# Optimization experiments

Measured on AMD Instinct MI355X. Metric: run time of the kernel, lower is better.

Reference implementation:

```python
import jax, jax.numpy as jnp
import numpy as np

N_EVENT = 100000
N_TRACE = 20000
E_EE = 1000000
E_ET = 500000
E_TE = 500000
D = 128          # embedding_dim == hidden_dim
OUT = 64         # output_dim
L = 3            # num_layers
NTYPES_EDGES = 3 # edge types
B = 64           # graphs per batch


def setup_inputs() -> dict:
    key = jax.random.key(0)
    ks = jax.random.split(key, 16)
    s = 1.0 / np.sqrt(D)
    inp = {
        "event_ids": jnp.arange(N_EVENT, dtype=jnp.int64 if jax.config.jax_enable_x64 else jnp.int32),
        "trace_ids": jnp.arange(N_TRACE, dtype=jnp.int64 if jax.config.jax_enable_x64 else jnp.int32),
        "e2e_src": jax.random.randint(ks[0], (E_EE,), 0, N_EVENT),
        "e2e_dst": jax.random.randint(ks[1], (E_EE,), 0, N_EVENT),
        "e2t_src": jax.random.randint(ks[2], (E_ET,), 0, N_EVENT),
        "e2t_dst": jax.random.randint(ks[3], (E_ET,), 0, N_TRACE),
        "t2e_src": jax.random.randint(ks[4], (E_TE,), 0, N_TRACE),
        "t2e_dst": jax.random.randint(ks[5], (E_TE,), 0, N_EVENT),
        "event_batch": jnp.sort(jax.random.randint(ks[6], (N_EVENT,), 0, B)),
        "trace_batch": jnp.sort(jax.random.randint(ks[7], (N_TRACE,), 0, B)),
        # learned parameters
        "emb_event": jax.random.normal(ks[8], (N_EVENT, D), jnp.float32),
        "emb_trace": jax.random.normal(ks[9], (N_TRACE, D), jnp.float32),
        # per-layer, per-edge-type SAGEConv weights: lin_l (neighbor, with bias), lin_r (root, no bias)
        "Wl": jax.random.normal(ks[10], (L, NTYPES_EDGES, D, D), jnp.float32) * s,
        "bl": jnp.zeros((L, NTYPES_EDGES, D), jnp.float32),
        "Wr": jax.random.normal(ks[11], (L, NTYPES_EDGES, D, D), jnp.float32) * s,
        # output MLP head
        "W1": jax.random.normal(ks[12], (D, D), jnp.float32) * s,
        "b1": jnp.zeros((D,), jnp.float32),
        "W2": jax.random.normal(ks[13], (OUT, D), jnp.float32) * s,
        "b2": jnp.zeros((OUT,), jnp.float32),
    }
    return inp


def reference(event_ids, trace_ids, e2e_src, e2e_dst, e2t_src, e2t_dst,
              t2e_src, t2e_dst, event_batch, trace_batch,
              emb_event, emb_trace, Wl, bl, Wr, W1, b1, W2, b2):
    def seg_mean(x_src, src, dst, n_dst):
        # mean-aggregate source features onto destination nodes (SAGEConv default aggr)
        s = jax.ops.segment_sum(x_src[src], dst, num_segments=n_dst)
        c = jax.ops.segment_sum(jnp.ones(dst.shape, x_src.dtype), dst, num_segments=n_dst)
        return s / jnp.maximum(c, 1.0)[:, None]

    # per-node-type embedding lookup
    x = {"event": emb_event[event_ids], "trace": emb_trace[trace_ids]}
    n = {"event": event_ids.shape[0], "trace": trace_ids.shape[0]}
    # edge types: (src_type, dst_type, src_idx, dst_idx), conv index matches Wl/bl/Wr axis 1
    edges = [
        ("event", "event", e2e_src, e2e_dst),
        ("event", "trace", e2t_src, e2t_dst),
        ("trace", "event", t2e_src, t2e_dst),
    ]
    n_layers = Wl.shape[0]
    for l in range(n_layers):
        new = {k: jnp.zeros((n[k], Wl.shape[-2]), x[k].dtype) for k in x}
        for i, (st, dt, s_idx, d_idx) in enumerate(edges):
            m = seg_mean(x[st], s_idx, d_idx, n[dt])
            # SAGEConv: lin_l(mean neighbors) + lin_r(root); HeteroConv aggr='sum' across edge types
            new[dt] = new[dt] + m @ Wl[l, i].T + bl[l, i] + x[dt] @ Wr[l, i].T
        x = new
    # global_add_pool per node type, then stack+sum over node types
    pooled = (jax.ops.segment_sum(x["event"], event_batch, num_segments=B)
              + jax.ops.segment_sum(x["trace"], trace_batch, num_segments=B))
    h = jax.nn.relu(pooled @ W1.T + b1)
    return h @ W2.T + b2
```

## Files before the change

### kernel.cpp

```cpp
#include <hip/hip_runtime.h>
#include <hip/hip_bf16.h>


#define D 128
#define NB 64
#define OUTD 64
#define NLAY 3
#define EPB 4096
#define BSH2 9

typedef __bf16 bf16;
typedef __bf16 bf16x4 __attribute__((ext_vector_type(4)));
typedef __bf16 bf16x8 __attribute__((ext_vector_type(8)));
typedef float  f32x16 __attribute__((ext_vector_type(16)));

#define LOAD16_TO_LDS(gp, lp) \
    __builtin_amdgcn_global_load_lds((const __attribute__((address_space(1))) void*)(gp), \
                                     (__attribute__((address_space(3))) void*)(lp), 16, 0, 0)

__global__ void gather_all(const float* __restrict__ embE, const int* __restrict__ idsE,
                           bf16* __restrict__ xE, int nE,
                           const float* __restrict__ embT, const int* __restrict__ idsT,
                           bf16* __restrict__ xT, int nT) {
    int idx = blockIdx.x * blockDim.x + threadIdx.x;
    const float* emb; const int* ids; bf16* x;
    int tE = nE * 32;
    if (idx < tE) { emb = embE; ids = idsE; x = xE; }
    else {
        idx -= tE;
        if (idx >= nT * 32) return;
        emb = embT; ids = idsT; x = xT;
    }
    int r = idx >> 5, v = idx & 31;
    float4 f = ((const float4*)(emb + (size_t)ids[r] * D))[v];
    bf16x4 o;
    o[0] = (bf16)f.x; o[1] = (bf16)f.y; o[2] = (bf16)f.z; o[3] = (bf16)f.w;
    ((bf16x4*)(x + (size_t)r * D))[v] = o;
}

__global__ void bkt_hist_all(const int* __restrict__ dEE, int nEE, int nbkEE, int nblkEE,
                             int* __restrict__ cntEE,
                             const int* __restrict__ dET, int nET, int nbkET, int nblkET,
                             int* __restrict__ cntET,
                             const int* __restrict__ dTE, int nTE, int nbkTE, int nblkTE,
                             int* __restrict__ cntTE) {
    __shared__ int h[256];
    int b = blockIdx.x;
    const int* dst; int E, nbk, nblk, lb; int* cnt;
    if (b < nblkEE) { dst = dEE; E = nEE; nbk = nbkEE; nblk = nblkEE; cnt = cntEE; lb = b; }
    else if (b < nblkEE + nblkET) { dst = dET; E = nET; nbk = nbkET; nblk = nblkET; cnt = cntET; lb = b - nblkEE; }
    else { dst = dTE; E = nTE; nbk = nbkTE; nblk = nblkTE; cnt = cntTE; lb = b - nblkEE - nblkET; }
    h[threadIdx.x] = 0;
    __syncthreads();
    int e0 = lb * EPB, e1 = min(e0 + EPB, E);
    for (int e = e0 + threadIdx.x; e < e1; e += 256) atomicAdd(&h[dst[e] >> BSH2], 1);
    __syncthreads();
    for (int k = threadIdx.x; k < nbk; k += 256) cnt[k * nblk + lb] = h[k];
}

__global__ void scan_p1_all(const int* __restrict__ dA, int* __restrict__ oA, int* __restrict__ sA, int nA,
                            const int* __restrict__ dB, int* __restrict__ oB, int* __restrict__ sB, int nB,
                            const int* __restrict__ dC, int* __restrict__ oC, int* __restrict__ sC, int nC) {
    int nbA = (nA + 1023) >> 10, nbB = (nB + 1023) >> 10;
    int b = blockIdx.x;
    const int* deg; int* off; int* bsum; int n; int lb;
    if (b < nbA) { deg = dA; off = oA; bsum = sA; n = nA; lb = b; }
    else if (b < nbA + nbB) { deg = dB; off = oB; bsum = sB; n = nB; lb = b - nbA; }
    else { deg = dC; off = oC; bsum = sC; n = nC; lb = b - nbA - nbB; }
    __shared__ int s[256];
    int t = threadIdx.x;
    int base = lb * 1024 + t * 4;
    int v[4];
    #pragma unroll
    for (int i = 0; i < 4; ++i) v[i] = (base + i < n) ? deg[base + i] : 0;
    int tot = v[0] + v[1] + v[2] + v[3];
    s[t] = tot;
    __syncthreads();
    for (int st = 1; st < 256; st <<= 1) {
        int x = (t >= st) ? s[t - st] : 0;
        __syncthreads();
        s[t] += x;
        __syncthreads();
    }
    int run = s[t] - tot;
    #pragma unroll
    for (int i = 0; i < 4; ++i) {
        if (base + i < n) off[base + i] = run;
        run += v[i];
    }
    if (t == 255) bsum[lb] = s[255];
}

__global__ void scan_p2_all(int* __restrict__ sA, int nbA,
                            int* __restrict__ sB, int nbB,
                            int* __restrict__ sC, int nbC) {
    int* bsum; int nb;
    if (blockIdx.x == 0) { bsum = sA; nb = nbA; }
    else if (blockIdx.x == 1) { bsum = sB; nb = nbB; }
    else { bsum = sC; nb = nbC; }
    __shared__ int s[256];
    int t = threadIdx.x;
    int v = (t < nb) ? bsum[t] : 0;
    s[t] = v;
    __syncthreads();
    for (int st = 1; st < 256; st <<= 1) {
        int x = (t >= st) ? s[t - st] : 0;
        __syncthreads();
        s[t] += x;
        __syncthreads();
    }
    if (t < nb) bsum[t] = s[t] - v;
    if (t == 0) bsum[nb] = s[255];
}

__global__ void scan_p3_all(int* __restrict__ oA, const int* __restrict__ sA, int nA,
                            int* __restrict__ oB, const int* __restrict__ sB, int nB,
                            int* __restrict__ oC, const int* __restrict__ sC, int nC) {
    int cbA = (nA + 255) >> 8, cbB = (nB + 255) >> 8;
    int b = blockIdx.x;
    int* off; const int* bsum; int n; int lb;
    if (b < cbA) { off = oA; bsum = sA; n = nA; lb = b; }
    else if (b < cbA + cbB) { off = oB; bsum = sB; n = nB; lb = b - cbA; }
    else { off = oC; bsum = sC; n = nC; lb = b - cbA - cbB; }
    int i = lb * 256 + threadIdx.x;
    if (i < n) off[i] += bsum[i >> 10];
    if (i == 0) off[n] = bsum[(n + 1023) >> 10];
}

__global__ void bkt_scatter_all(const int* __restrict__ sEE, const int* __restrict__ dEE,
                                int nEE, int nbkEE, int nblkEE, const int* __restrict__ SEE,
                                int2* __restrict__ ebEE,
                                const int* __restrict__ sET, const int* __restrict__ dET,
                                int nET, int nbkET, int nblkET, const int* __restrict__ SET,
                                int2* __restrict__ ebET,
                                const int* __restrict__ sTE, const int* __restrict__ dTE,
                                int nTE, int nbkTE, int nblkTE, const int* __restrict__ STE,
                                int2* __restrict__ ebTE) {
    __shared__ int cu[256];
    int b = blockIdx.x;
    const int* src; const int* dst; const int* S; int2* eb; int E, nbk, nblk, lb;
    if (b < nblkEE) { src = sEE; dst = dEE; S = SEE; eb = ebEE; E = nEE; nbk = nbkEE; nblk = nblkEE; lb = b; }
    else if (b < nblkEE + nblkET) { src = sET; dst = dET; S = SET; eb = ebET; E = nET; nbk = nbkET; nblk = nblkET; lb = b - nblkEE; }
    else { src = sTE; dst = dTE; S = STE; eb = ebTE; E = nTE; nbk = nbkTE; nblk = nblkTE; lb = b - nblkEE - nblkET; }
    for (int k = threadIdx.x; k < nbk; k += 256) cu[k] = S[k * nblk + lb];
    __syncthreads();
    int e0 = lb * EPB, e1 = min(e0 + EPB, E);
    for (int e = e0 + threadIdx.x; e < e1; e += 256) {
        int s = src[e], d = dst[e];
        int p = atomicAdd(&cu[d >> BSH2], 1);
        eb[p] = make_int2(s, d);
    }
}

__global__ void csr_build_all(const int2* __restrict__ ebEE, const int* __restrict__ SEE,
                              int nbkEE, int nblkEE, int ndEE,
                              int* __restrict__ offEE, int* __restrict__ adjEE,
                              const int2* __restrict__ ebET, const int* __restrict__ SET,
                              int nbkET, int nblkET, int ndET,
                              int* __restrict__ offET, int* __restrict__ adjET,
                              const int2* __restrict__ ebTE, const int* __restrict__ STE,
                              int nbkTE, int nblkTE, int ndTE,
                              int* __restrict__ offTE, int* __restrict__ adjTE) {
    __shared__ int h[512];
    __shared__ int ps[256];
    __shared__ int cc[512];
    int b = blockIdx.x;
    const int2* eb; const int* S; int nbk, nblk, ndst, k; int* off; int* adj;
    if (b < nbkEE) { eb = ebEE; S = SEE; nbk = nbkEE; nblk = nblkEE; ndst = ndEE; off = offEE; adj = adjEE; k = b; }
    else if (b < nbkEE + nbkET) { eb = ebET; S = SET; nbk = nbkET; nblk = nblkET; ndst = ndET; off = offET; adj = adjET; k = b - nbkEE; }
    else { eb = ebTE; S = STE; nbk = nbkTE; nblk = nblkTE; ndst = ndTE; off = offTE; adj = adjTE; k = b - nbkEE - nbkET; }
    int base = S[k * nblk];
    int end  = (k == nbk - 1) ? S[nbk * nblk] : S[(k + 1) * nblk];
    int d0 = k << BSH2;
    int t = threadIdx.x;
    h[t] = 0; h[t + 256] = 0;
    __syncthreads();
    for (int j = base + t; j < end; j += 256) atomicAdd(&h[eb[j].y - d0], 1);
    __syncthreads();
    int a0 = h[2 * t], a1 = h[2 * t + 1];
    ps[t] = a0 + a1;
    __syncthreads();
    for (int st = 1; st < 256; st <<= 1) {
        int x = (t >= st) ? ps[t - st] : 0;
        __syncthreads();
        ps[t] += x;
        __syncthreads();
    }
    int pe = ps[t] - (a0 + a1);
    int o0 = base + pe, o1 = base + pe + a0;
    cc[2 * t] = o0; cc[2 * t + 1] = o1;
    int nd = min(512, ndst - d0);
    if (2 * t < nd) off[d0 + 2 * t] = o0;
    if (2 * t + 1 < nd) off[d0 + 2 * t + 1] = o1;
    if (t == 0 && k == nbk - 1) off[ndst] = end;
    __syncthreads();
    for (int j = base + t; j < end; j += 256) {
        int2 e = eb[j];
        int p = atomicAdd(&cc[e.y - d0], 1);
        adj[p] = e.x;
    }
}

__global__ void agg_all(const bf16* __restrict__ xE, const bf16* __restrict__ xT,
                        const int* __restrict__ offEE, const int* __restrict__ adjEE,
                        const int* __restrict__ offTE, const int* __restrict__ adjTE,
                        const int* __restrict__ offET, const int* __restrict__ adjET,
                        bf16* __restrict__ mEE, bf16* __restrict__ mTE, bf16* __restrict__ mET,
                        int nE, int nT) {
    int gw = (blockIdx.x * blockDim.x + threadIdx.x) >> 6;
    int lane = threadIdx.x & 63;
    int qE = (nE + 3) >> 2, qT = (nT + 3) >> 2;
    const bf16* xsrc; const int* off; const int* adj; bf16* out; int ndst;
    if (gw < qE) { xsrc = xE; off = offEE; adj = adjEE; out = mEE; ndst = nE; }
    else if (gw < 2 * qE) { gw -= qE; xsrc = xT; off = offTE; adj = adjTE; out = mTE; ndst = nE; }
    else {
        gw -= 2 * qE;
        if (gw >= qT) return;
        xsrc = xE; off = offET; adj = adjET; out = mET; ndst = nT;
    }
    int sub = lane >> 4;
    int sl  = lane & 15;
    int row = gw * 4 + sub;
    if (row >= ndst) row = ndst - 1;
    int s0 = off[row], s1 = off[row + 1];
    float a[8] = {};
    int j = s0;
    for (; j + 8 <= s1; j += 8) {
        int ii[8];
        #pragma unroll
        for (int u = 0; u < 8; ++u) ii[u] = adj[j + u];
        bf16x8 v[8];
        #pragma unroll
        for (int u = 0; u < 8; ++u) v[u] = ((const bf16x8*)(xsrc + (size_t)ii[u] * D))[sl];
        #pragma unroll
        for (int u = 0; u < 8; ++u)
            #pragma unroll
            for (int e = 0; e < 8; ++e) a[e] += (float)v[u][e];
    }
    for (; j + 4 <= s1; j += 4) {
        int i0 = adj[j], i1 = adj[j + 1], i2 = adj[j + 2], i3 = adj[j + 3];
        bf16x8 v0 = ((const bf16x8*)(xsrc + (size_t)i0 * D))[sl];
        bf16x8 v1 = ((const bf16x8*)(xsrc + (size_t)i1 * D))[sl];
        bf16x8 v2 = ((const bf16x8*)(xsrc + (size_t)i2 * D))[sl];
        bf16x8 v3 = ((const bf16x8*)(xsrc + (size_t)i3 * D))[sl];
        #pragma unroll
        for (int e = 0; e < 8; ++e)
            a[e] += (float)v0[e] + (float)v1[e] + (float)v2[e] + (float)v3[e];
    }
    for (; j < s1; ++j) {
        int i0 = adj[j];
        bf16x8 v0 = ((const bf16x8*)(xsrc + (size_t)i0 * D))[sl];
        #pragma unroll
        for (int e = 0; e < 8; ++e) a[e] += (float)v0[e];
    }
    float inv = 1.0f / fmaxf((float)(s1 - s0), 1.0f);
    bf16x8 o;
    #pragma unroll
    for (int e = 0; e < 8; ++e) o[e] = (bf16)(a[e] * inv);
    ((bf16x8*)(out + (size_t)row * D))[sl] = o;
}

__global__ void prep_weights_packed(const float* __restrict__ Wl, const float* __restrict__ Wr,
                                    bf16* __restrict__ wbuf) {
    int idx = blockIdx.x * blockDim.x + threadIdx.x;
    if (idx >= NLAY * 5 * 2048) return;
    int l = idx / (5 * 2048);
    int rem = idx - l * 5 * 2048;
    int mat = rem >> 11;
    int q = rem & 2047;
    int lane = q & 63, t = (q >> 6) & 7, w = q >> 9;
    int r = w * 32 + (lane & 31);
    int c = t * 16 + (lane >> 5) * 8;
    size_t l3 = (size_t)l * 3;
    const float* s0;
    const float* s1 = nullptr;
    switch (mat) {
        case 0: s0 = Wl + (l3 + 0) * D * D; break;
        case 1: s0 = Wl + (l3 + 2) * D * D; break;
        case 2: s0 = Wr + (l3 + 0) * D * D; s1 = Wr + (l3 + 2) * D * D; break;
        case 3: s0 = Wl + (l3 + 1) * D * D; break;
        default: s0 = Wr + (l3 + 1) * D * D; break;
    }
    bf16x8 hi, lo;
    #pragma unroll
    for (int e = 0; e < 8; ++e) {
        float v = s0[r * D + c + e];
        if (s1) v += s1[r * D + c + e];
        bf16 h = (bf16)v;
        hi[e] = h;
        lo[e] = (bf16)(v - (float)h);
    }
    bf16* base = wbuf + (size_t)l * 10 * D * D;
    ((bf16x8*)(base + (size_t)(2 * mat) * D * D))[q] = hi;
    ((bf16x8*)(base + (size_t)(2 * mat + 1) * D * D))[q] = lo;
}

__global__ void prep_bias(const float* __restrict__ bl, float* __restrict__ bbuf) {
    int idx = blockIdx.x * blockDim.x + threadIdx.x;
    if (idx >= NLAY * D) return;
    int l = idx >> 7, o = idx & (D - 1);
    bbuf[l * 2 * D + o]     = bl[(size_t)(l * 3 + 0) * D + o] + bl[(size_t)(l * 3 + 2) * D + o];
    bbuf[l * 2 * D + D + o] = bl[(size_t)(l * 3 + 1) * D + o];
}

__device__ __forceinline__ void gemm_body(const bf16* A0, const bf16* A1, const bf16* A2,
                                          const bf16* Wp, const float* bias, bf16* out,
                                          int M, int nm, int row0, bf16* As) {
    int tid = threadIdx.x;
    int wave = tid >> 6, lane = tid & 63;
    int m = lane & 31, half = lane >> 5;

    f32x16 acc[2];
    #pragma unroll
    for (int rt = 0; rt < 2; ++rt)
        #pragma unroll
        for (int i = 0; i < 16; ++i) acc[rt][i] = 0.f;

    const bf16* Aptr[3] = {A0, A1, A2};
    #pragma unroll
    for (int s = 0; s < 3; ++s) {
        if (s >= nm) break;
        if (s) __syncthreads();
        const bf16* Amat = Aptr[s];
        #pragma unroll
        for (int p = 0; p < 4; ++p) {
            int si = p * 256 + tid;
            int r = si >> 4, u = si & 15;
            int gr = row0 + r; if (gr >= M) gr = M - 1;
            int gc = (u ^ (r & 15)) * 8;
            LOAD16_TO_LDS(Amat + (size_t)gr * D + gc, As + (size_t)(p * 4 + wave) * 512);
        }
        const bf16* wph = Wp + (size_t)(2 * s) * D * D + ((size_t)wave * 512 + lane) * 8;
        const bf16* wpl = wph + D * D;
        bf16x8 bh_c  = *(const bf16x8*)(wph);
        bf16x8 blo_c = *(const bf16x8*)(wpl);
        __syncthreads();

        #pragma unroll 1
        for (int t = 0; t < 8; ++t) {
            bf16x8 bh_n, blo_n;
            if (t < 7) {
                bh_n  = *(const bf16x8*)(wph + (t + 1) * 512);
                blo_n = *(const bf16x8*)(wpl + (t + 1) * 512);
            }
            bf16x8 af[2];
            #pragma unroll
            for (int rt = 0; rt < 2; ++rt) {
                int r = rt * 32 + m;
                int c = t * 2 + half;
                af[rt] = *(const bf16x8*)(As + ((size_t)r * 16 + (c ^ (r & 15))) * 8);
            }
            acc[0] = __builtin_amdgcn_mfma_f32_32x32x16_bf16(af[0], bh_c,  acc[0], 0, 0, 0);
            acc[1] = __builtin_amdgcn_mfma_f32_32x32x16_bf16(af[1], bh_c,  acc[1], 0, 0, 0);
            acc[0] = __builtin_amdgcn_mfma_f32_32x32x16_bf16(af[0], blo_c, acc[0], 0, 0, 0);
            acc[1] = __builtin_amdgcn_mfma_f32_32x32x16_bf16(af[1], blo_c, acc[1], 0, 0, 0);
            bh_c = bh_n; blo_c = blo_n;
        }
    }

    int col = wave * 32 + m;
    float bv = bias[col];
    #pragma unroll
    for (int rt = 0; rt < 2; ++rt) {
        #pragma unroll
        for (int r = 0; r < 16; ++r) {
            int row = row0 + rt * 32 + (r & 3) + 8 * (r >> 2) + 4 * half;
            if (row < M) out[(size_t)row * D + col] = (bf16)(acc[rt][r] + bv);
        }
    }
}

__global__ __launch_bounds__(256) void gemm_all(const bf16* __restrict__ eA0, const bf16* __restrict__ eA1,
                                                const bf16* __restrict__ eA2, const bf16* __restrict__ eW,
                                                const float* __restrict__ eB, bf16* __restrict__ eOut,
                                                int Me, int bE,
                                                const bf16* __restrict__ tA0, const bf16* __restrict__ tA1,
                                                const bf16* __restrict__ tW, const float* __restrict__ tB,
                                                bf16* __restrict__ tOut, int Mt) {
    __shared__ bf16 As[64 * 128];
    if ((int)blockIdx.x < bE)
        gemm_body(eA0, eA1, eA2, eW, eB, eOut, Me, 3, blockIdx.x * 64, As);
    else
        gemm_body(tA0, tA1, (const bf16*)nullptr, tW, tB, tOut, Mt, 2,
                  ((int)blockIdx.x - bE) * 64, As);
}

__global__ void pool_m_all(const bf16* __restrict__ m_ee, const bf16* __restrict__ m_te,
                           const bf16* __restrict__ xE, const bf16* __restrict__ m_et,
                           const bf16* __restrict__ xT,
                           const int* __restrict__ bEv, const int* __restrict__ bTr,
                           int nE, int nT, int pbE, int pbT,
                           float* __restrict__ pooled5, int* __restrict__ cntE,
                           int* __restrict__ cntT) {
    int c = threadIdx.x;
    int blk = blockIdx.x;
    const bf16* x; const int* batch; int n, r0, s;
    if (blk < 3 * pbE) {
        s = blk / pbE; int lb = blk - s * pbE;
        x = (s == 0) ? m_ee : (s == 1) ? m_te : xE;
        batch = bEv; n = nE; r0 = lb * 64;
    } else {
        int q = blk - 3 * pbE;
        s = 3 + q / pbT; int lb = q - (s - 3) * pbT;
        x = (s == 3) ? m_et : xT;
        batch = bTr; n = nT; r0 = lb * 64;
    }
    int r1 = min(r0 + 64, n);
    if (r0 >= r1) return;
    float* P = pooled5 + (size_t)s * NB * D;
    int* cnt = (s == 2) ? cntE : (s == 4) ? cntT : nullptr;
    int cur = batch[r0];
    float acc = 0.f;
    int run = 0;
    for (int r = r0; r < r1; ++r) {
        int b = batch[r];
        if (b != cur) {
            atomicAdd(&P[cur * D + c], acc);
            if (cnt && c == 0) atomicAdd(&cnt[cur], run);
            acc = 0.f; run = 0; cur = b;
        }
        acc += (float)x[(size_t)r * D + c];
        run++;
    }
    atomicAdd(&P[cur * D + c], acc);
    if (cnt && c == 0) atomicAdd(&cnt[cur], run);
}

__global__ void tail_kernel(const float* __restrict__ pooled5, const int* __restrict__ cntE,
                            const int* __restrict__ cntT,
                            const float* __restrict__ Wl, const float* __restrict__ Wr,
                            const float* __restrict__ bl,
                            const float* __restrict__ W1, const float* __restrict__ b1,
                            const float* __restrict__ W2, const float* __restrict__ b2,
                            float* __restrict__ out) {
    __shared__ float p5[5][D];
    __shared__ float hp[D];
    __shared__ float hh[D];
    int b = blockIdx.x, t = threadIdx.x;
    #pragma unroll
    for (int s = 0; s < 5; ++s) p5[s][t] = pooled5[(size_t)(s * NB + b) * D + t];
    __syncthreads();
    float ce = (float)cntE[b], ct = (float)cntT[b];
    float s = ce * (bl[6 * D + t] + bl[8 * D + t]) + ct * bl[7 * D + t];
    const float* w0  = Wl + (size_t)6 * D * D + (size_t)t * D;
    const float* w2  = Wl + (size_t)8 * D * D + (size_t)t * D;
    const float* wr0 = Wr + (size_t)6 * D * D + (size_t)t * D;
    const float* wr2 = Wr + (size_t)8 * D * D + (size_t)t * D;
    const float* w1m = Wl + (size_t)7 * D * D + (size_t)t * D;
    const float* wr1 = Wr + (size_t)7 * D * D + (size_t)t * D;
    #pragma unroll 4
    for (int k = 0; k < D; ++k)
        s += p5[0][k] * w0[k] + p5[1][k] * w2[k] + p5[2][k] * (wr0[k] + wr2[k])
           + p5[3][k] * w1m[k] + p5[4][k] * wr1[k];
    hp[t] = s;
    __syncthreads();
    float s1 = b1[t];
    const float* u = W1 + (size_t)t * D;
    #pragma unroll 4
    for (int k = 0; k < D; ++k) s1 += hp[k] * u[k];
    hh[t] = fmaxf(s1, 0.f);
    __syncthreads();
    if (t < OUTD) {
        float s2 = b2[t];
        const float* v = W2 + (size_t)t * D;
        #pragma unroll 4
        for (int k = 0; k < D; ++k) s2 += hh[k] * v[k];
        out[b * OUTD + t] = s2;
    }
}

extern "C" void kernel_launch(void* const* d_in, const int* in_sizes, int n_in,
                              void* d_out, int out_size, void* d_ws, size_t ws_size,
                              hipStream_t stream) {
    const int* event_ids   = (const int*)d_in[0];
    const int* trace_ids   = (const int*)d_in[1];
    const int* e2e_src     = (const int*)d_in[2];
    const int* e2e_dst     = (const int*)d_in[3];
    const int* e2t_src     = (const int*)d_in[4];
    const int* e2t_dst     = (const int*)d_in[5];
    const int* t2e_src     = (const int*)d_in[6];
    const int* t2e_dst     = (const int*)d_in[7];
    const int* event_batch = (const int*)d_in[8];
    const int* trace_batch = (const int*)d_in[9];
    const float* emb_event = (const float*)d_in[10];
    const float* emb_trace = (const float*)d_in[11];
    const float* Wl        = (const float*)d_in[12];
    const float* bl        = (const float*)d_in[13];
    const float* Wr        = (const float*)d_in[14];
    const float* W1        = (const float*)d_in[15];
    const float* b1        = (const float*)d_in[16];
    const float* W2        = (const float*)d_in[17];
    const float* b2        = (const float*)d_in[18];

    const int NE = in_sizes[0];
    const int NT = in_sizes[1];
    const int EE = in_sizes[2];
    const int ET = in_sizes[4];
    const int TE = in_sizes[6];

    const int nbkEE = (NE + 511) >> BSH2, nblkEE = (EE + EPB - 1) / EPB;
    const int nbkET = (NT + 511) >> BSH2, nblkET = (ET + EPB - 1) / EPB;
    const int nbkTE = (NE + 511) >> BSH2, nblkTE = (TE + EPB - 1) / EPB;
    const int cEE = nbkEE * nblkEE, cET = nbkET * nblkET, cTE = nbkTE * nblkTE;

    size_t cur = 0;
    auto alloc = [&](size_t bytes) -> void* {
        cur = (cur + 255) & ~(size_t)255;
        void* p = (char*)d_ws + cur;
        cur += bytes;
        return p;
    };
    bf16* x_event   = (bf16*)alloc((size_t)NE * D * 2);
    bf16* x_trace   = (bf16*)alloc((size_t)NT * D * 2);
    bf16* nx_event  = (bf16*)alloc((size_t)NE * D * 2);
    bf16* nx_trace  = (bf16*)alloc((size_t)NT * D * 2);
    bf16* m_ee      = (bf16*)alloc((size_t)NE * D * 2);
    bf16* m_te      = (bf16*)alloc((size_t)NE * D * 2);
    bf16* m_et      = (bf16*)alloc((size_t)NT * D * 2);
    bf16* wbuf      = (bf16*)alloc((size_t)NLAY * 10 * D * D * 2);
    float* bbuf     = (float*)alloc((size_t)NLAY * 2 * D * 4);
    size_t zInts = (size_t)5 * NB * D + 2 * NB;
    int* zbase  = (int*)alloc(zInts * 4);
    float* pooled5 = (float*)zbase;
    int* cntE = (int*)(pooled5 + 5 * NB * D);
    int* cntT = cntE + NB;
    int* off_ee = (int*)alloc((size_t)(NE + 1) * 4);
    int* adj_ee = (int*)alloc((size_t)EE * 4);
    int* off_et = (int*)alloc((size_t)(NT + 1) * 4);
    int* adj_et = (int*)alloc((size_t)ET * 4);
    int* off_te = (int*)alloc((size_t)(NE + 1) * 4);
    int* adj_te = (int*)alloc((size_t)TE * 4);
    int* cnt_ee = (int*)alloc((size_t)cEE * 4);
    int* S_ee   = (int*)alloc((size_t)(cEE + 1) * 4);
    int* cnt_et = (int*)alloc((size_t)cET * 4);
    int* S_et   = (int*)alloc((size_t)(cET + 1) * 4);
    int* cnt_te = (int*)alloc((size_t)cTE * 4);
    int* S_te   = (int*)alloc((size_t)(cTE + 1) * 4);
    int* bsum_ee = (int*)alloc(((size_t)(cEE + 1023) / 1024 + 1) * 4);
    int* bsum_et = (int*)alloc(((size_t)(cET + 1023) / 1024 + 1) * 4);
    int* bsum_te = (int*)alloc(((size_t)(cTE + 1023) / 1024 + 1) * 4);
    int2* eb_ee = (int2*)m_ee;
    int2* eb_et = (int2*)m_te;
    int2* eb_te = (int2*)m_et;
    (void)ws_size; (void)n_in; (void)out_size;

    hipMemsetAsync(zbase, 0, zInts * 4, stream);

    gather_all<<<((NE + NT) * 32 + 255) / 256, 256, 0, stream>>>(
        emb_event, event_ids, x_event, NE, emb_trace, trace_ids, x_trace, NT);

    prep_weights_packed<<<(NLAY * 5 * 2048 + 255) / 256, 256, 0, stream>>>(Wl, Wr, wbuf);
    prep_bias<<<(NLAY * D + 255) / 256, 256, 0, stream>>>(bl, bbuf);

    bkt_hist_all<<<nblkEE + nblkET + nblkTE, 256, 0, stream>>>(
        e2e_dst, EE, nbkEE, nblkEE, cnt_ee,
        e2t_dst, ET, nbkET, nblkET, cnt_et,
        t2e_dst, TE, nbkTE, nblkTE, cnt_te);
    const int nb1 = (cEE + 1023) >> 10, nb2 = (cET + 1023) >> 10, nb3 = (cTE + 1023) >> 10;
    scan_p1_all<<<nb1 + nb2 + nb3, 256, 0, stream>>>(
        cnt_ee, S_ee, bsum_ee, cEE, cnt_et, S_et, bsum_et, cET, cnt_te, S_te, bsum_te, cTE);
    scan_p2_all<<<3, 256, 0, stream>>>(bsum_ee, nb1, bsum_et, nb2, bsum_te, nb3);
    scan_p3_all<<<((cEE + 255) >> 8) + ((cET + 255) >> 8) + ((cTE + 255) >> 8), 256, 0, stream>>>(
        S_ee, bsum_ee, cEE, S_et, bsum_et, cET, S_te, bsum_te, cTE);
    bkt_scatter_all<<<nblkEE + nblkET + nblkTE, 256, 0, stream>>>(
        e2e_src, e2e_dst, EE, nbkEE, nblkEE, S_ee, eb_ee,
        e2t_src, e2t_dst, ET, nbkET, nblkET, S_et, eb_et,
        t2e_src, t2e_dst, TE, nbkTE, nblkTE, S_te, eb_te);
    csr_build_all<<<nbkEE + nbkET + nbkTE, 256, 0, stream>>>(
        eb_ee, S_ee, nbkEE, nblkEE, NE, off_ee, adj_ee,
        eb_et, S_et, nbkET, nblkET, NT, off_et, adj_et,
        eb_te, S_te, nbkTE, nblkTE, NE, off_te, adj_te);

    const int qE = (NE + 3) >> 2, qT = (NT + 3) >> 2;
    const int aggBlocks = (2 * qE + qT + 3) / 4;
    const int bE = (NE + 63) / 64, bT = (NT + 63) / 64;
    for (int l = 0; l < NLAY; ++l) {
        agg_all<<<aggBlocks, 256, 0, stream>>>(x_event, x_trace,
                                               off_ee, adj_ee, off_te, adj_te, off_et, adj_et,
                                               m_ee, m_te, m_et, NE, NT);
        if (l < NLAY - 1) {
            const bf16* wl_ev = wbuf + (size_t)l * 10 * D * D;
            const bf16* wl_tr = wl_ev + (size_t)6 * D * D;
            const float* be = bbuf + (size_t)l * 2 * D;
            const float* bt = be + D;
            gemm_all<<<bE + bT, 256, 0, stream>>>(m_ee, m_te, x_event, wl_ev, be, nx_event, NE, bE,
                                                  m_et, x_trace, wl_tr, bt, nx_trace, NT);
            bf16* t;
            t = x_event; x_event = nx_event; nx_event = t;
            t = x_trace; x_trace = nx_trace; nx_trace = t;
        }
    }

    const int pbE = (NE + 63) / 64, pbT = (NT + 63) / 64;
    pool_m_all<<<3 * pbE + 2 * pbT, D, 0, stream>>>(m_ee, m_te, x_event, m_et, x_trace,
                                                    event_batch, trace_batch, NE, NT, pbE, pbT,
                                                    pooled5, cntE, cntT);
    tail_kernel<<<NB, D, 0, stream>>>(pooled5, cntE, cntT, Wl, Wr, bl,
                                      W1, b1, W2, b2, (float*)d_out);
}
```

Measured before the change: 602.3 us.

## Fuse front-end prep kernels, merge scan phases, double-buffer GEMM weights, enlarge pool chunks

Folds the embedding gather, weight packing and bias prep into one launch, and merges scan phases 2 and 3 so that every block redundantly rescans the block sums. This is meant to cut kernel-launch count and the serial dependencies between tiny kernels. The GEMM inner loop is fully unrolled with a two-deep register prefetch of weight fragments, and its launch bounds now request 8 blocks per multiprocessor. Pooling chunks grow from 64 to 256 rows to reduce atomics. The costs are redundant scan work in each block and possible register pressure under the tighter launch bounds.

```diff
diff --git a/kernel.cpp b/kernel.cpp
--- a/kernel.cpp
+++ b/kernel.cpp
@@ -8,6 +8,7 @@
 #define NLAY 3
 #define EPB 4096
 #define BSH2 9
+#define PCH 256
 
 typedef __bf16 bf16;
 typedef __bf16 bf16x4 __attribute__((ext_vector_type(4)));
@@ -18,24 +19,69 @@
     __builtin_amdgcn_global_load_lds((const __attribute__((address_space(1))) void*)(gp), \
                                      (__attribute__((address_space(3))) void*)(lp), 16, 0, 0)
 
-__global__ void gather_all(const float* __restrict__ embE, const int* __restrict__ idsE,
-                           bf16* __restrict__ xE, int nE,
-                           const float* __restrict__ embT, const int* __restrict__ idsT,
-                           bf16* __restrict__ xT, int nT) {
-    int idx = blockIdx.x * blockDim.x + threadIdx.x;
-    const float* emb; const int* ids; bf16* x;
-    int tE = nE * 32;
-    if (idx < tE) { emb = embE; ids = idsE; x = xE; }
-    else {
-        idx -= tE;
-        if (idx >= nT * 32) return;
-        emb = embT; ids = idsT; x = xT;
-    }
-    int r = idx >> 5, v = idx & 31;
-    float4 f = ((const float4*)(emb + (size_t)ids[r] * D))[v];
-    bf16x4 o;
-    o[0] = (bf16)f.x; o[1] = (bf16)f.y; o[2] = (bf16)f.z; o[3] = (bf16)f.w;
-    ((bf16x4*)(x + (size_t)r * D))[v] = o;
+__global__ void front_all(const float* __restrict__ embE, const int* __restrict__ idsE,
+                          bf16* __restrict__ xE, int nE,
+                          const float* __restrict__ embT, const int* __restrict__ idsT,
+                          bf16* __restrict__ xT, int nT,
+                          const float* __restrict__ Wl, const float* __restrict__ Wr,
+                          const float* __restrict__ bl,
+                          bf16* __restrict__ wbuf, float* __restrict__ bbuf,
+                          int nGather) {
+    int b = blockIdx.x;
+    if (b < nGather) {
+        int idx = b * 256 + threadIdx.x;
+        const float* emb; const int* ids; bf16* x;
+        int tE = nE * 32;
+        if (idx < tE) { emb = embE; ids = idsE; x = xE; }
+        else {
+            idx -= tE;
+            if (idx >= nT * 32) return;
+            emb = embT; ids = idsT; x = xT;
+        }
+        int r = idx >> 5, v = idx & 31;
+        float4 f = ((const float4*)(emb + (size_t)ids[r] * D))[v];
+        bf16x4 o;
+        o[0] = (bf16)f.x; o[1] = (bf16)f.y; o[2] = (bf16)f.z; o[3] = (bf16)f.w;
+        ((bf16x4*)(x + (size_t)r * D))[v] = o;
+    } else if (b < nGather + 120) {
+        int idx = (b - nGather) * 256 + threadIdx.x;
+        if (idx >= NLAY * 5 * 2048) return;
+        int l = idx / (5 * 2048);
+        int rem = idx - l * 5 * 2048;
+        int mat = rem >> 11;
+        int q = rem & 2047;
+        int lane = q & 63, t = (q >> 6) & 7, w = q >> 9;
+        int r = w * 32 + (lane & 31);
+        int c = t * 16 + (lane >> 5) * 8;
+        size_t l3 = (size_t)l * 3;
+        const float* s0;
+        const float* s1 = nullptr;
+        switch (mat) {
+            case 0: s0 = Wl + (l3 + 0) * D * D; break;
+            case 1: s0 = Wl + (l3 + 2) * D * D; break;
+            case 2: s0 = Wr + (l3 + 0) * D * D; s1 = Wr + (l3 + 2) * D * D; break;
+            case 3: s0 = Wl + (l3 + 1) * D * D; break;
+            default: s0 = Wr + (l3 + 1) * D * D; break;
+        }
+        bf16x8 hi, lo;
+        #pragma unroll
+        for (int e = 0; e < 8; ++e) {
+            float v = s0[r * D + c + e];
+            if (s1) v += s1[r * D + c + e];
+            bf16 h = (bf16)v;
+            hi[e] = h;
+            lo[e] = (bf16)(v - (float)h);
+        }
+        bf16* base = wbuf + (size_t)l * 10 * D * D;
+        ((bf16x8*)(base + (size_t)(2 * mat) * D * D))[q] = hi;
+        ((bf16x8*)(base + (size_t)(2 * mat + 1) * D * D))[q] = lo;
+    } else {
+        int idx = (b - nGather - 120) * 256 + threadIdx.x;
+        if (idx >= NLAY * D) return;
+        int l = idx >> 7, o = idx & (D - 1);
+        bbuf[l * 2 * D + o]     = bl[(size_t)(l * 3 + 0) * D + o] + bl[(size_t)(l * 3 + 2) * D + o];
+        bbuf[l * 2 * D + D + o] = bl[(size_t)(l * 3 + 1) * D + o];
+    }
 }
 
 __global__ void bkt_hist_all(const int* __restrict__ dEE, int nEE, int nbkEE, int nblkEE,
@@ -91,40 +137,33 @@
     if (t == 255) bsum[lb] = s[255];
 }
 
-__global__ void scan_p2_all(int* __restrict__ sA, int nbA,
-                            int* __restrict__ sB, int nbB,
-                            int* __restrict__ sC, int nbC) {
-    int* bsum; int nb;
-    if (blockIdx.x == 0) { bsum = sA; nb = nbA; }
-    else if (blockIdx.x == 1) { bsum = sB; nb = nbB; }
-    else { bsum = sC; nb = nbC; }
-    __shared__ int s[256];
-    int t = threadIdx.x;
-    int v = (t < nb) ? bsum[t] : 0;
-    s[t] = v;
-    __syncthreads();
-    for (int st = 1; st < 256; st <<= 1) {
-        int x = (t >= st) ? s[t - st] : 0;
-        __syncthreads();
-        s[t] += x;
-        __syncthreads();
-    }
-    if (t < nb) bsum[t] = s[t] - v;
-    if (t == 0) bsum[nb] = s[255];
-}
-
-__global__ void scan_p3_all(int* __restrict__ oA, const int* __restrict__ sA, int nA,
-                            int* __restrict__ oB, const int* __restrict__ sB, int nB,
-                            int* __restrict__ oC, const int* __restrict__ sC, int nC) {
+__global__ void scan_p23_all(int* __restrict__ oA, const int* __restrict__ sA, int nA,
+                             int* __restrict__ oB, const int* __restrict__ sB, int nB,
+                             int* __restrict__ oC, const int* __restrict__ sC, int nC) {
     int cbA = (nA + 255) >> 8, cbB = (nB + 255) >> 8;
     int b = blockIdx.x;
     int* off; const int* bsum; int n; int lb;
     if (b < cbA) { off = oA; bsum = sA; n = nA; lb = b; }
     else if (b < cbA + cbB) { off = oB; bsum = sB; n = nB; lb = b - cbA; }
     else { off = oC; bsum = sC; n = nC; lb = b - cbA - cbB; }
-    int i = lb * 256 + threadIdx.x;
-    if (i < n) off[i] += bsum[i >> 10];
-    if (i == 0) off[n] = bsum[(n + 1023) >> 10];
+    __shared__ int s[256];
+    __shared__ int ex[256];
+    int nb = (n + 1023) >> 10;
+    int t = threadIdx.x;
+    int v = (t < nb) ? bsum[t] : 0;
+    s[t] = v;
+    __syncthreads();
+    for (int st = 1; st < 256; st <<= 1) {
+        int x = (t >= st) ? s[t - st] : 0;
+        __syncthreads();
+        s[t] += x;
+        __syncthreads();
+    }
+    ex[t] = s[t] - v;
+    __syncthreads();
+    int i = lb * 256 + t;
+    if (i < n) off[i] += ex[i >> 10];
+    if (i == 0) off[n] = s[nb - 1];
 }
 
 __global__ void bkt_scatter_all(const int* __restrict__ sEE, const int* __restrict__ dEE,
@@ -260,49 +299,6 @@
     ((bf16x8*)(out + (size_t)row * D))[sl] = o;
 }
 
-__global__ void prep_weights_packed(const float* __restrict__ Wl, const float* __restrict__ Wr,
-                                    bf16* __restrict__ wbuf) {
-    int idx = blockIdx.x * blockDim.x + threadIdx.x;
-    if (idx >= NLAY * 5 * 2048) return;
-    int l = idx / (5 * 2048);
-    int rem = idx - l * 5 * 2048;
-    int mat = rem >> 11;
-    int q = rem & 2047;
-    int lane = q & 63, t = (q >> 6) & 7, w = q >> 9;
-    int r = w * 32 + (lane & 31);
-    int c = t * 16 + (lane >> 5) * 8;
-    size_t l3 = (size_t)l * 3;
-    const float* s0;
-    const float* s1 = nullptr;
-    switch (mat) {
-        case 0: s0 = Wl + (l3 + 0) * D * D; break;
-        case 1: s0 = Wl + (l3 + 2) * D * D; break;
-        case 2: s0 = Wr + (l3 + 0) * D * D; s1 = Wr + (l3 + 2) * D * D; break;
-        case 3: s0 = Wl + (l3 + 1) * D * D; break;
-        default: s0 = Wr + (l3 + 1) * D * D; break;
-    }
-    bf16x8 hi, lo;
-    #pragma unroll
-    for (int e = 0; e < 8; ++e) {
-        float v = s0[r * D + c + e];
-        if (s1) v += s1[r * D + c + e];
-        bf16 h = (bf16)v;
-        hi[e] = h;
-        lo[e] = (bf16)(v - (float)h);
-    }
-    bf16* base = wbuf + (size_t)l * 10 * D * D;
-    ((bf16x8*)(base + (size_t)(2 * mat) * D * D))[q] = hi;
-    ((bf16x8*)(base + (size_t)(2 * mat + 1) * D * D))[q] = lo;
-}
-
-__global__ void prep_bias(const float* __restrict__ bl, float* __restrict__ bbuf) {
-    int idx = blockIdx.x * blockDim.x + threadIdx.x;
-    if (idx >= NLAY * D) return;
-    int l = idx >> 7, o = idx & (D - 1);
-    bbuf[l * 2 * D + o]     = bl[(size_t)(l * 3 + 0) * D + o] + bl[(size_t)(l * 3 + 2) * D + o];
-    bbuf[l * 2 * D + D + o] = bl[(size_t)(l * 3 + 1) * D + o];
-}
-
 __device__ __forceinline__ void gemm_body(const bf16* A0, const bf16* A1, const bf16* A2,
                                           const bf16* Wp, const float* bias, bf16* out,
                                           int M, int nm, int row0, bf16* As) {
@@ -332,16 +328,19 @@
         }
         const bf16* wph = Wp + (size_t)(2 * s) * D * D + ((size_t)wave * 512 + lane) * 8;
         const bf16* wpl = wph + D * D;
-        bf16x8 bh_c  = *(const bf16x8*)(wph);
-        bf16x8 blo_c = *(const bf16x8*)(wpl);
-        __syncthreads();
-
-        #pragma unroll 1
+        bf16x8 bh0 = *(const bf16x8*)(wph);
+        bf16x8 bl0 = *(const bf16x8*)(wpl);
+        bf16x8 bh1 = *(const bf16x8*)(wph + 512);
+        bf16x8 bl1 = *(const bf16x8*)(wpl + 512);
+        __syncthreads();
+
+        #pragma unroll
         for (int t = 0; t < 8; ++t) {
-            bf16x8 bh_n, blo_n;
-            if (t < 7) {
-                bh_n  = *(const bf16x8*)(wph + (t + 1) * 512);
-                blo_n = *(const bf16x8*)(wpl + (t + 1) * 512);
+            bf16x8 bhc = (t & 1) ? bh1 : bh0;
+            bf16x8 blc = (t & 1) ? bl1 : bl0;
+            if (t < 6) {
+                if (t & 1) { bh1 = *(const bf16x8*)(wph + (t + 2) * 512); bl1 = *(const bf16x8*)(wpl + (t + 2) * 512); }
+                else       { bh0 = *(const bf16x8*)(wph + (t + 2) * 512); bl0 = *(const bf16x8*)(wpl + (t + 2) * 512); }
             }
             bf16x8 af[2];
             #pragma unroll
@@ -350,11 +349,10 @@
                 int c = t * 2 + half;
                 af[rt] = *(const bf16x8*)(As + ((size_t)r * 16 + (c ^ (r & 15))) * 8);
             }
-            acc[0] = __builtin_amdgcn_mfma_f32_32x32x16_bf16(af[0], bh_c,  acc[0], 0, 0, 0);
-            acc[1] = __builtin_amdgcn_mfma_f32_32x32x16_bf16(af[1], bh_c,  acc[1], 0, 0, 0);
-            acc[0] = __builtin_amdgcn_mfma_f32_32x32x16_bf16(af[0], blo_c, acc[0], 0, 0, 0);
-            acc[1] = __builtin_amdgcn_mfma_f32_32x32x16_bf16(af[1], blo_c, acc[1], 0, 0, 0);
-            bh_c = bh_n; blo_c = blo_n;
+            acc[0] = __builtin_amdgcn_mfma_f32_32x32x16_bf16(af[0], bhc, acc[0], 0, 0, 0);
+            acc[1] = __builtin_amdgcn_mfma_f32_32x32x16_bf16(af[1], bhc, acc[1], 0, 0, 0);
+            acc[0] = __builtin_amdgcn_mfma_f32_32x32x16_bf16(af[0], blc, acc[0], 0, 0, 0);
+            acc[1] = __builtin_amdgcn_mfma_f32_32x32x16_bf16(af[1], blc, acc[1], 0, 0, 0);
         }
     }
 
@@ -370,13 +368,13 @@
     }
 }
 
-__global__ __launch_bounds__(256) void gemm_all(const bf16* __restrict__ eA0, const bf16* __restrict__ eA1,
-                                                const bf16* __restrict__ eA2, const bf16* __restrict__ eW,
-                                                const float* __restrict__ eB, bf16* __restrict__ eOut,
-                                                int Me, int bE,
-                                                const bf16* __restrict__ tA0, const bf16* __restrict__ tA1,
-                                                const bf16* __restrict__ tW, const float* __restrict__ tB,
-                                                bf16* __restrict__ tOut, int Mt) {
+__global__ __launch_bounds__(256, 8) void gemm_all(const bf16* __restrict__ eA0, const bf16* __restrict__ eA1,
+                                                   const bf16* __restrict__ eA2, const bf16* __restrict__ eW,
+                                                   const float* __restrict__ eB, bf16* __restrict__ eOut,
+                                                   int Me, int bE,
+                                                   const bf16* __restrict__ tA0, const bf16* __restrict__ tA1,
+                                                   const bf16* __restrict__ tW, const float* __restrict__ tB,
+                                                   bf16* __restrict__ tOut, int Mt) {
     __shared__ bf16 As[64 * 128];
     if ((int)blockIdx.x < bE)
         gemm_body(eA0, eA1, eA2, eW, eB, eOut, Me, 3, blockIdx.x * 64, As);
@@ -398,14 +396,14 @@
     if (blk < 3 * pbE) {
         s = blk / pbE; int lb = blk - s * pbE;
         x = (s == 0) ? m_ee : (s == 1) ? m_te : xE;
-        batch = bEv; n = nE; r0 = lb * 64;
+        batch = bEv; n = nE; r0 = lb * PCH;
     } else {
         int q = blk - 3 * pbE;
         s = 3 + q / pbT; int lb = q - (s - 3) * pbT;
         x = (s == 3) ? m_et : xT;
-        batch = bTr; n = nT; r0 = lb * 64;
-    }
-    int r1 = min(r0 + 64, n);
+        batch = bTr; n = nT; r0 = lb * PCH;
+    }
+    int r1 = min(r0 + PCH, n);
     if (r0 >= r1) return;
     float* P = pooled5 + (size_t)s * NB * D;
     int* cnt = (s == 2) ? cntE : (s == 4) ? cntT : nullptr;
@@ -546,11 +544,10 @@
 
     hipMemsetAsync(zbase, 0, zInts * 4, stream);
 
-    gather_all<<<((NE + NT) * 32 + 255) / 256, 256, 0, stream>>>(
-        emb_event, event_ids, x_event, NE, emb_trace, trace_ids, x_trace, NT);
-
-    prep_weights_packed<<<(NLAY * 5 * 2048 + 255) / 256, 256, 0, stream>>>(Wl, Wr, wbuf);
-    prep_bias<<<(NLAY * D + 255) / 256, 256, 0, stream>>>(bl, bbuf);
+    const int nGather = ((NE + NT) * 32 + 255) / 256;
+    front_all<<<nGather + 122, 256, 0, stream>>>(
+        emb_event, event_ids, x_event, NE, emb_trace, trace_ids, x_trace, NT,
+        Wl, Wr, bl, wbuf, bbuf, nGather);
 
     bkt_hist_all<<<nblkEE + nblkET + nblkTE, 256, 0, stream>>>(
         e2e_dst, EE, nbkEE, nblkEE, cnt_ee,
@@ -559,8 +556,7 @@
     const int nb1 = (cEE + 1023) >> 10, nb2 = (cET + 1023) >> 10, nb3 = (cTE + 1023) >> 10;
     scan_p1_all<<<nb1 + nb2 + nb3, 256, 0, stream>>>(
         cnt_ee, S_ee, bsum_ee, cEE, cnt_et, S_et, bsum_et, cET, cnt_te, S_te, bsum_te, cTE);
-    scan_p2_all<<<3, 256, 0, stream>>>(bsum_ee, nb1, bsum_et, nb2, bsum_te, nb3);
-    scan_p3_all<<<((cEE + 255) >> 8) + ((cET + 255) >> 8) + ((cTE + 255) >> 8), 256, 0, stream>>>(
+    scan_p23_all<<<((cEE + 255) >> 8) + ((cET + 255) >> 8) + ((cTE + 255) >> 8), 256, 0, stream>>>(
         S_ee, bsum_ee, cEE, S_et, bsum_et, cET, S_te, bsum_te, cTE);
     bkt_scatter_all<<<nblkEE + nblkET + nblkTE, 256, 0, stream>>>(
         e2e_src, e2e_dst, EE, nbkEE, nblkEE, S_ee, eb_ee,
@@ -591,7 +587,7 @@
         }
     }
 
-    const int pbE = (NE + 63) / 64, pbT = (NT + 63) / 64;
+    const int pbE = (NE + PCH - 1) / PCH, pbT = (NT + PCH - 1) / PCH;
     pool_m_all<<<3 * pbE + 2 * pbT, D, 0, stream>>>(m_ee, m_te, x_event, m_et, x_trace,
                                                     event_batch, trace_batch, NE, NT, pbE, pbT,
                                                     pooled5, cntE, cntT);
```

Result: slower. 697.5 us (+15.8%).
